# Kernel optimization log

Measured on AMD Instinct MI355X. Metric: run time of the kernel, lower is better.

Reference implementation:

```python
import jax, jax.numpy as jnp
import numpy as np

D_MODEL, N_LEVELS, N_HEADS, N_POINTS = 256, 4, 8, 4
HEAD_DIM = D_MODEL // N_HEADS
SPATIAL = [(100, 100), (50, 50), (25, 25), (13, 13)]  # (H, W) per level
BATCH = 2


def setup_inputs() -> dict:
    key = jax.random.key(0)
    ks = jax.random.split(key, 10)
    len_in = sum(h * w for h, w in SPATIAL)
    n, lq = BATCH, len_in
    s = 0.02
    mlp = N_HEADS * N_LEVELS * N_POINTS
    starts = np.cumsum([0] + [h * w for h, w in SPATIAL])[:-1]
    return {
        "query": jax.random.normal(ks[0], (n, lq, D_MODEL), jnp.float32),
        "reference_points": jax.random.uniform(ks[1], (n, lq, N_LEVELS, 2), jnp.float32),
        "input_flatten": jax.random.normal(ks[2], (n, len_in, D_MODEL), jnp.float32),
        "input_spatial_shapes": jnp.array(SPATIAL, dtype=jnp.int32),
        "input_level_start_index": jnp.array(starts, dtype=jnp.int32),
        "Wv": jax.random.normal(ks[3], (D_MODEL, D_MODEL), jnp.float32) * s,
        "bv": jnp.zeros((D_MODEL,), jnp.float32),
        "Woff": jax.random.normal(ks[4], (D_MODEL, mlp * 2), jnp.float32) * s,
        "boff": jax.random.normal(ks[5], (mlp * 2,), jnp.float32) * s,
        "Wattn": jax.random.normal(ks[6], (D_MODEL, mlp), jnp.float32) * s,
        "battn": jnp.zeros((mlp,), jnp.float32),
        "Wout": jax.random.normal(ks[7], (D_MODEL, D_MODEL), jnp.float32) * s,
        "bout": jnp.zeros((D_MODEL,), jnp.float32),
    }


def _ms_deform_attn_core(value, spatial_shapes, loc, aw):
    """value [N,S,M,D]; loc [N,Lq,M,L,P,2] in [0,1]; aw [N,Lq,M,L,P] -> [N,Lq,M*D].
    Faithful to F.grid_sample(mode='bilinear', padding_mode='zeros', align_corners=False)."""
    n, lq, m, L, p, _ = loc.shape
    d = value.shape[-1]
    out = jnp.zeros((n, m, lq, d), value.dtype)
    gather = jax.vmap(jax.vmap(lambda v, i: v[i]))  # vmap over N and M
    start = 0
    for lvl, (H, W) in enumerate(spatial_shapes):
        v = value[:, start:start + H * W].transpose(0, 2, 1, 3)  # [N,M,HW,D]
        start += H * W
        # align_corners=False: grid g=2*loc-1 -> pixel = ((g+1)*size-1)/2 = loc*size-0.5
        x = loc[:, :, :, lvl, :, 0] * W - 0.5  # [N,Lq,M,P]
        y = loc[:, :, :, lvl, :, 1] * H - 0.5
        x0 = jnp.floor(x)
        y0 = jnp.floor(y)
        wx = x - x0
        wy = y - y0
        x0i = x0.astype(jnp.int32)
        y0i = y0.astype(jnp.int32)
        samp = jnp.zeros((n, m, lq * p, d), value.dtype)
        for dy, wyc in ((0, 1.0 - wy), (1, wy)):
            for dx, wxc in ((0, 1.0 - wx), (1, wx)):
                xi = x0i + dx
                yi = y0i + dy
                valid = (xi >= 0) & (xi < W) & (yi >= 0) & (yi < H)  # zeros padding
                idx = jnp.clip(yi, 0, H - 1) * W + jnp.clip(xi, 0, W - 1)
                idx = idx.transpose(0, 2, 1, 3).reshape(n, m, lq * p)
                w = (wxc * wyc * valid).transpose(0, 2, 1, 3).reshape(n, m, lq * p)
                samp = samp + gather(v, idx) * w[..., None]
        samp = samp.reshape(n, m, lq, p, d)
        aw_l = aw[:, :, :, lvl, :].transpose(0, 2, 1, 3)  # [N,M,Lq,P]
        out = out + (samp * aw_l[..., None]).sum(3)
    return out.transpose(0, 2, 1, 3).reshape(n, lq, m * d)


def reference(query, reference_points, input_flatten, input_spatial_shapes,
              input_level_start_index, Wv, bv, Woff, boff, Wattn, battn, Wout, bout):
    n, lq, _ = query.shape
    m, L, p = N_HEADS, N_LEVELS, N_POINTS
    shapes = np.asarray(input_spatial_shapes)  # concrete/static [L,2] = (H,W)
    value = (input_flatten @ Wv + bv).reshape(n, -1, m, HEAD_DIM)
    off = (query @ Woff + boff).reshape(n, lq, m, L, p, 2)
    aw = jax.nn.softmax((query @ Wattn + battn).reshape(n, lq, m, L * p), axis=-1)
    aw = aw.reshape(n, lq, m, L, p)
    norm = jnp.asarray(shapes[:, ::-1].astype(np.float32))  # [L,2] = (W,H)
    loc = reference_points[:, :, None, :, None, :] + off / norm[None, None, None, :, None, :]
    out = _ms_deform_attn_core(value, [tuple(s) for s in shapes.tolist()], loc, aw)
    return out @ Wout + bout
```

## Files before the change

### kernel.cpp

```cpp
#include <hip/hip_runtime.h>
#include <hip/hip_bf16.h>

#define NB    2
#define LQ    13294
#define DM    256
#define NH    8
#define HD    32
#define NL    4
#define NP    4
#define ROWS  (NB*LQ)

#define OFF_VALUE 0u
#define OFF_TMP   13613056u
#define OFF_OFFS  27226112u
#define OFF_AWL   54452224u
#define OFF_WT    61258752u
#define OFF_FLAG  61717504u

#define WT_WV    0
#define WT_WOFF  65536
#define WT_WATTN 131072
#define WT_WOUT  163840

#define NPANEL   831
#define NBLK_VAL (NPANEL*4)
#define NBLK_FUS (NPANEL*6)
#define NBLK_IN  (NBLK_VAL+NBLK_FUS)
#define NGRP_IN  ((NBLK_IN+3)/4)
#define NGRP_OUT (NBLK_VAL/4)

typedef __attribute__((ext_vector_type(8))) short short8;
typedef __attribute__((ext_vector_type(4))) float floatx4;

static __device__ __forceinline__ float blo(int u)  { return __uint_as_float(((unsigned)u) << 16); }
static __device__ __forceinline__ float bhif(int u) { return __uint_as_float(((unsigned)u) & 0xffff0000u); }

static __device__ __forceinline__ int pack_bf2(float a, float b) {
    __hip_bfloat162 h(__float2bfloat16(a), __float2bfloat16(b));
    int u; __builtin_memcpy(&u, &h, 4); return u;
}

static __device__ __forceinline__ int xcd_swz(int b, int nblk) {
    const int q = nblk >> 3, r = nblk & 7;
    const int x = b & 7, i = b >> 3;
    return x * q + min(x, r) + i;
}

__global__ void sniff_k(const unsigned int* __restrict__ q, int* __restrict__ flag) {
    const int t = threadIdx.x;
    int hits = 0;
#pragma unroll
    for (int i = 0; i < 4; ++i) {
        unsigned lo = q[t * 4 + i] & 0xffffu;
        unsigned e  = (lo >> 7) & 0xffu;
        if ((e >= 110u && e <= 132u) || lo == 0u) ++hits;
    }
#pragma unroll
    for (int s = 1; s < 64; s <<= 1) hits += __shfl_xor(hits, s);
    if (t == 0) *flag = (hits > 160) ? 1 : 0;
}

__global__ __launch_bounds__(256) void trans_k(
    const void* __restrict__ s0, const void* __restrict__ s1,
    const void* __restrict__ s2, const void* __restrict__ s3,
    short* __restrict__ wt, const int* __restrict__ flagp)
{
    const int flag = *flagp;
    const int z = blockIdx.z;
    const void* src = (z == 0) ? s0 : (z == 1) ? s1 : (z == 2) ? s2 : s3;
    short* dst = wt + ((z == 0) ? WT_WV : (z == 1) ? WT_WOFF : (z == 2) ? WT_WATTN : WT_WOUT);
    const int N = (z == 2) ? 128 : 256;
    const int n0 = blockIdx.x * 32, k0 = blockIdx.y * 32;
    if (n0 >= N) return;

    __shared__ short tile[32 * 36];
    const int t = threadIdx.x;
    const int r = t >> 3, c4 = (t & 7) * 4;
    if (flag) {
        const short* sp = (const short*)src + (k0 + r) * N + n0 + c4;
        *(short4*)&tile[r * 36 + c4] = *(const short4*)sp;
    } else {
        const float* sp = (const float*)src + (k0 + r) * N + n0 + c4;
        float4 v = *(const float4*)sp;
        short4 o;
        o.x = (short)(pack_bf2(v.x, v.x) & 0xffff);
        o.y = (short)(pack_bf2(v.y, v.y) & 0xffff);
        o.z = (short)(pack_bf2(v.z, v.z) & 0xffff);
        o.w = (short)(pack_bf2(v.w, v.w) & 0xffff);
        *(short4*)&tile[r * 36 + c4] = o;
    }
    __syncthreads();
    const int nn = t >> 3, r4 = (t & 7) * 4;
    short4 o;
    o.x = tile[(r4 + 0) * 36 + nn];
    o.y = tile[(r4 + 1) * 36 + nn];
    o.z = tile[(r4 + 2) * 36 + nn];
    o.w = tile[(r4 + 3) * 36 + nn];
    *(short4*)&dst[(n0 + nn) * 256 + k0 + r4] = o;
}

static __device__ __forceinline__ short8 ldA_f32(const float* p) {
    float4 f0 = *(const float4*)p, f1 = *(const float4*)(p + 4);
    int4 q; q.x = pack_bf2(f0.x, f0.y); q.y = pack_bf2(f0.z, f0.w);
            q.z = pack_bf2(f1.x, f1.y); q.w = pack_bf2(f1.z, f1.w);
    short8 r; __builtin_memcpy(&r, &q, 16); return r;
}

static __device__ __forceinline__ void wgemm_body(
    const void* __restrict__ A, const short* __restrict__ Wt,
    const void* __restrict__ bias, const void* __restrict__ bias2,
    void* __restrict__ C, void* __restrict__ C2,
    const int M, const int Nn, const bool a_bf, const int c_mode,
    const int flag, const int bn_t, const int p_t, const int lane)
{
    const int qd = lane >> 4, ln = lane & 15;
    const int bm = p_t * 32, bn = bn_t * 64;

    const int ar0 = min(bm + ln, M - 1);
    const int ar1 = min(bm + 16 + ln, M - 1);
    const short* Ab = (const short*)A;
    const float* Af = (const float*)A;

    floatx4 acc[2][4];
#pragma unroll
    for (int i = 0; i < 2; ++i)
#pragma unroll
        for (int j = 0; j < 4; ++j) acc[i][j] = floatx4{0.f, 0.f, 0.f, 0.f};

    if (a_bf) {
#pragma unroll 2
        for (int kk = 0; kk < 8; ++kk) {
            const int k0 = kk * 32 + qd * 8;
            short8 af0 = *(const short8*)(Ab + ar0 * 256 + k0);
            short8 af1 = *(const short8*)(Ab + ar1 * 256 + k0);
            short8 bf[4];
#pragma unroll
            for (int j = 0; j < 4; ++j)
                bf[j] = *(const short8*)(Wt + (bn + j * 16 + ln) * 256 + k0);
#pragma unroll
            for (int j = 0; j < 4; ++j) {
                acc[0][j] = __builtin_amdgcn_mfma_f32_16x16x32_bf16(af0, bf[j], acc[0][j], 0, 0, 0);
                acc[1][j] = __builtin_amdgcn_mfma_f32_16x16x32_bf16(af1, bf[j], acc[1][j], 0, 0, 0);
            }
        }
    } else {
#pragma unroll 2
        for (int kk = 0; kk < 8; ++kk) {
            const int k0 = kk * 32 + qd * 8;
            short8 af0 = ldA_f32(Af + ar0 * 256 + k0);
            short8 af1 = ldA_f32(Af + ar1 * 256 + k0);
            short8 bf[4];
#pragma unroll
            for (int j = 0; j < 4; ++j)
                bf[j] = *(const short8*)(Wt + (bn + j * 16 + ln) * 256 + k0);
#pragma unroll
            for (int j = 0; j < 4; ++j) {
                acc[0][j] = __builtin_amdgcn_mfma_f32_16x16x32_bf16(af0, bf[j], acc[0][j], 0, 0, 0);
                acc[1][j] = __builtin_amdgcn_mfma_f32_16x16x32_bf16(af1, bf[j], acc[1][j], 0, 0, 0);
            }
        }
    }

#pragma unroll
    for (int j = 0; j < 4; ++j) {
        const int col = bn + j * 16 + ln;
        float bj;
        if (c_mode == 3 && col >= 256) {
            if (flag) bj = __bfloat162float(((const __hip_bfloat16*)bias2)[col - 256]);
            else      bj = ((const float*)bias2)[col - 256];
        } else {
            if (flag) bj = __bfloat162float(((const __hip_bfloat16*)bias)[col]);
            else      bj = ((const float*)bias)[col];
        }
#pragma unroll
        for (int i = 0; i < 2; ++i) {
#pragma unroll
            for (int r = 0; r < 4; ++r) {
                const int row = bm + i * 16 + qd * 4 + r;
                if (row >= M) continue;
                const float v = acc[i][j][r] + bj;
                if (c_mode == 0)      ((__hip_bfloat16*)C)[row * Nn + col] = __float2bfloat16(v);
                else if (c_mode == 1) ((float*)C)[row * Nn + col] = v;
                else if (c_mode == 2) {
                    if (flag) ((__hip_bfloat16*)C)[row * Nn + col] = __float2bfloat16(v);
                    else      ((float*)C)[row * Nn + col] = v;
                } else {
                    if (col < 256) ((float*)C)[row * 256 + col] = v;
                    else           ((__hip_bfloat16*)C2)[row * 128 + col - 256] = __float2bfloat16(v);
                }
            }
        }
    }
}

__global__ __launch_bounds__(256) void wgemm_in_k(
    const void* __restrict__ flat, const void* __restrict__ query,
    const short* __restrict__ wt,
    const void* __restrict__ bv, const void* __restrict__ boff,
    const void* __restrict__ battn,
    void* __restrict__ value, void* __restrict__ offsb, void* __restrict__ awl,
    const int* __restrict__ flagp)
{
    const int flag = *flagp;
    const bool a_bf = (flag != 0);
    const int w = xcd_swz(blockIdx.x, NGRP_IN) * 4 + (threadIdx.x >> 6);
    if (w >= NBLK_IN) return;
    const int lane = threadIdx.x & 63;
    if (w < NBLK_VAL) {
        wgemm_body(flat, wt + WT_WV, bv, nullptr, value, nullptr,
                   ROWS, 256, a_bf, 0, flag, w & 3, w >> 2, lane);
    } else {
        const int w2 = w - NBLK_VAL;
        wgemm_body(query, wt + WT_WOFF, boff, battn, offsb, awl,
                   ROWS, 384, a_bf, 3, flag, w2 % 6, w2 / 6, lane);
    }
}

__global__ __launch_bounds__(256) void wgemm_out_k(
    const void* __restrict__ tmp, const short* __restrict__ wt,
    const void* __restrict__ bout, void* __restrict__ dout,
    const int* __restrict__ flagp)
{
    const int flag = *flagp;
    const int w = xcd_swz(blockIdx.x, NGRP_OUT) * 4 + (threadIdx.x >> 6);
    const int lane = threadIdx.x & 63;
    wgemm_body(tmp, wt + WT_WOUT, bout, nullptr, dout, nullptr,
               ROWS, 256, true, 2, flag, w & 3, w >> 2, lane);
}

__global__ __launch_bounds__(256) void sampler_k(
    const void* __restrict__ refp, const short* __restrict__ value,
    const float* __restrict__ offs, const short* __restrict__ awl,
    short* __restrict__ tmp, const int* __restrict__ flagp)
{
    const int flag = *flagp;
    const int wq = threadIdx.x >> 6;
    const int nq = blockIdx.x * 4 + wq;
    const int lane = threadIdx.x & 63;
    const int h = lane >> 3, u = lane & 7;
    const int n = (nq >= LQ) ? 1 : 0;

    __shared__ int2 recs[4][16][9][5];

    const int lg = *(const int*)(awl + nq * 128 + h * 16 + u * 2);
    float l0 = blo(lg), l1 = bhif(lg);
    float m = fmaxf(l0, l1);
    m = fmaxf(m, __shfl_xor(m, 1));
    m = fmaxf(m, __shfl_xor(m, 2));
    m = fmaxf(m, __shfl_xor(m, 4));
    float e0 = __expf(l0 - m), e1 = __expf(l1 - m);
    float s = e0 + e1;
    s += __shfl_xor(s, 1);
    s += __shfl_xor(s, 2);
    s += __shfl_xor(s, 4);
    const float inv = 1.f / s;
    const float w0 = e0 * inv, w1 = e1 * inv;

    const float4 of = *(const float4*)(offs + nq * 256 + h * 32 + u * 4);

    float rxl, ryl;
    if (flag) {
        const int rr = *(const int*)((const short*)refp + nq * 8 + (u & 3) * 2);
        rxl = blo(rr); ryl = bhif(rr);
    } else {
        const float* rp = (const float*)refp + nq * 8 + (u & 3) * 2;
        rxl = rp[0]; ryl = rp[1];
    }

    const int l = u >> 1;
    const int Wl = (0x0D193264 >> (l * 8)) & 0xff;
    const int St = (l == 0) ? 0 : (l == 1) ? 10000 : (l == 2) ? 12500 : 13125;
    const int rowbase = n * LQ + St;
    const float Wf = (float)Wl;
    const float rx = __shfl(rxl, h * 8 + l);
    const float ry = __shfl(ryl, h * 8 + l);

#pragma unroll
    for (int j = 0; j < 2; ++j) {
        const float ox = j ? of.z : of.x;
        const float oy = j ? of.w : of.y;
        const float wa = j ? w1 : w0;
        const float px = fmaf(rx, Wf, ox) - 0.5f;
        const float py = fmaf(ry, Wf, oy) - 0.5f;
        const float x0f = floorf(px), y0f = floorf(py);
        const float wx = px - x0f, wy = py - y0f;
        const int x0 = (int)x0f, y0 = (int)y0f;
        const float wxc[2] = {1.f - wx, wx};
        const float wyc[2] = {1.f - wy, wy};
#pragma unroll
        for (int dy = 0; dy < 2; ++dy) {
#pragma unroll
            for (int dx = 0; dx < 2; ++dx) {
                const int xi = x0 + dx, yi = y0 + dy;
                const bool vld = ((unsigned)xi < (unsigned)Wl) & ((unsigned)yi < (unsigned)Wl);
                int row = rowbase + yi * Wl + xi;
                row = vld ? row : rowbase;
                recs[wq][u * 2 + j][h][dy * 2 + dx] =
                    make_int2(row << 9, __float_as_int(vld ? wa * wxc[dx] * wyc[dy] : 0.f));
            }
        }
    }

    __syncthreads();

    const int laneoff = h * 64 + u * 8;
    const char* vb = (const char*)value;
    float a0 = 0.f, a1 = 0.f, a2 = 0.f, a3 = 0.f;

    int2  rA[8], rB[8];
    float wA[8], wB[8];

#define CHUNK(RW, WW, kk)                                                 \
    _Pragma("unroll")                                                     \
    for (int j = 0; j < 8; ++j) {                                         \
        const int2 rr = recs[wq][(kk) * 2 + (j >> 2)][h][j & 3];          \
        WW[j] = __int_as_float(rr.y);                                     \
        RW[j] = *(const int2*)(vb + (unsigned)(rr.x + laneoff));          \
    }
#define EAT(RW, WW)                                                       \
    _Pragma("unroll")                                                     \
    for (int j = 0; j < 8; ++j) {                                         \
        a0 = fmaf(WW[j], blo(RW[j].x),  a0);                              \
        a1 = fmaf(WW[j], bhif(RW[j].x), a1);                              \
        a2 = fmaf(WW[j], blo(RW[j].y),  a2);                              \
        a3 = fmaf(WW[j], bhif(RW[j].y), a3);                              \
    }

    CHUNK(rA, wA, 0)
    CHUNK(rB, wB, 1)
    EAT(rA, wA)  CHUNK(rA, wA, 2)
    EAT(rB, wB)  CHUNK(rB, wB, 3)
    EAT(rA, wA)  CHUNK(rA, wA, 4)
    EAT(rB, wB)  CHUNK(rB, wB, 5)
    EAT(rA, wA)  CHUNK(rA, wA, 6)
    EAT(rB, wB)  CHUNK(rB, wB, 7)
    EAT(rA, wA)
    EAT(rB, wB)
#undef CHUNK
#undef EAT

    int2 o;
    o.x = pack_bf2(a0, a1);
    o.y = pack_bf2(a2, a3);
    *(int2*)(tmp + nq * 256 + h * 32 + u * 4) = o;
}

extern "C" void kernel_launch(void* const* d_in, const int* in_sizes, int n_in,
                              void* d_out, int out_size, void* d_ws, size_t ws_size,
                              hipStream_t stream)
{
    const void* query  = d_in[0];
    const void* refpts = d_in[1];
    const void* flat   = d_in[2];
    const void* Wv     = d_in[5];
    const void* bv     = d_in[6];
    const void* Woff   = d_in[7];
    const void* boff   = d_in[8];
    const void* Wattn  = d_in[9];
    const void* battn  = d_in[10];
    const void* Wout   = d_in[11];
    const void* bout   = d_in[12];

    char* ws = (char*)d_ws;
    short* value = (short*)(ws + OFF_VALUE);
    short* tmp   = (short*)(ws + OFF_TMP);
    float* offsb = (float*)(ws + OFF_OFFS);
    short* awl   = (short*)(ws + OFF_AWL);
    short* wt    = (short*)(ws + OFF_WT);
    int*   flagp = (int*)(ws + OFF_FLAG);

    sniff_k<<<1, 64, 0, stream>>>((const unsigned int*)query, flagp);
    trans_k<<<dim3(8, 8, 4), 256, 0, stream>>>(Wv, Woff, Wattn, Wout, wt, flagp);
    wgemm_in_k<<<NGRP_IN, 256, 0, stream>>>(flat, query, wt, bv, boff, battn,
                                            value, offsb, awl, flagp);
    sampler_k<<<ROWS / 4, 256, 0, stream>>>(refpts, value, offsb, awl, tmp, flagp);
    wgemm_out_k<<<NGRP_OUT, 256, 0, stream>>>(tmp, wt, bout, d_out, flagp);
}
```

Measured before the change: 269.0 us.

## Stage GEMM epilogues through LDS for coalesced 16-byte row-panel stores

Each block in the input and output projection GEMMs now covers a full 32-row panel, with its four waves splitting the columns. Wave-to-tile mapping is reorganized so one block covers all columns of 32 rows. Results plus bias are written to shared memory first, then copied to global memory as contiguous int4 stores. Previously each lane did scattered 2- or 4-byte stores. This cuts uncoalesced write traffic at the cost of LDS usage (up to 40 KB per block), which may lower occupancy, plus an extra barrier.

```diff
diff --git a/kernel.cpp b/kernel.cpp
--- a/kernel.cpp
+++ b/kernel.cpp
@@ -23,11 +23,8 @@
 #define WT_WOUT  163840
 
 #define NPANEL   831
-#define NBLK_VAL (NPANEL*4)
-#define NBLK_FUS (NPANEL*6)
-#define NBLK_IN  (NBLK_VAL+NBLK_FUS)
-#define NGRP_IN  ((NBLK_IN+3)/4)
-#define NGRP_OUT (NBLK_VAL/4)
+#define NGRID_IN (NPANEL*2)
+#define NGRID_OUT NPANEL
 
 typedef __attribute__((ext_vector_type(8))) short short8;
 typedef __attribute__((ext_vector_type(4))) float floatx4;
@@ -106,26 +103,22 @@
     short8 r; __builtin_memcpy(&r, &q, 16); return r;
 }
 
-static __device__ __forceinline__ void wgemm_body(
+template<int NJ>
+static __device__ __forceinline__ void wg_compute(
     const void* __restrict__ A, const short* __restrict__ Wt,
-    const void* __restrict__ bias, const void* __restrict__ bias2,
-    void* __restrict__ C, void* __restrict__ C2,
-    const int M, const int Nn, const bool a_bf, const int c_mode,
-    const int flag, const int bn_t, const int p_t, const int lane)
+    const bool a_bf, const int bm, const int bn, const int lane,
+    floatx4 (&acc)[2][NJ])
 {
     const int qd = lane >> 4, ln = lane & 15;
-    const int bm = p_t * 32, bn = bn_t * 64;
-
-    const int ar0 = min(bm + ln, M - 1);
-    const int ar1 = min(bm + 16 + ln, M - 1);
+    const int ar0 = min(bm + ln, ROWS - 1);
+    const int ar1 = min(bm + 16 + ln, ROWS - 1);
     const short* Ab = (const short*)A;
     const float* Af = (const float*)A;
 
-    floatx4 acc[2][4];
 #pragma unroll
     for (int i = 0; i < 2; ++i)
 #pragma unroll
-        for (int j = 0; j < 4; ++j) acc[i][j] = floatx4{0.f, 0.f, 0.f, 0.f};
+        for (int j = 0; j < NJ; ++j) acc[i][j] = floatx4{0.f, 0.f, 0.f, 0.f};
 
     if (a_bf) {
 #pragma unroll 2
@@ -133,12 +126,12 @@
             const int k0 = kk * 32 + qd * 8;
             short8 af0 = *(const short8*)(Ab + ar0 * 256 + k0);
             short8 af1 = *(const short8*)(Ab + ar1 * 256 + k0);
-            short8 bf[4];
-#pragma unroll
-            for (int j = 0; j < 4; ++j)
+            short8 bf[NJ];
+#pragma unroll
+            for (int j = 0; j < NJ; ++j)
                 bf[j] = *(const short8*)(Wt + (bn + j * 16 + ln) * 256 + k0);
 #pragma unroll
-            for (int j = 0; j < 4; ++j) {
+            for (int j = 0; j < NJ; ++j) {
                 acc[0][j] = __builtin_amdgcn_mfma_f32_16x16x32_bf16(af0, bf[j], acc[0][j], 0, 0, 0);
                 acc[1][j] = __builtin_amdgcn_mfma_f32_16x16x32_bf16(af1, bf[j], acc[1][j], 0, 0, 0);
             }
@@ -149,45 +142,14 @@
             const int k0 = kk * 32 + qd * 8;
             short8 af0 = ldA_f32(Af + ar0 * 256 + k0);
             short8 af1 = ldA_f32(Af + ar1 * 256 + k0);
-            short8 bf[4];
-#pragma unroll
-            for (int j = 0; j < 4; ++j)
+            short8 bf[NJ];
+#pragma unroll
+            for (int j = 0; j < NJ; ++j)
                 bf[j] = *(const short8*)(Wt + (bn + j * 16 + ln) * 256 + k0);
 #pragma unroll
-            for (int j = 0; j < 4; ++j) {
+            for (int j = 0; j < NJ; ++j) {
                 acc[0][j] = __builtin_amdgcn_mfma_f32_16x16x32_bf16(af0, bf[j], acc[0][j], 0, 0, 0);
                 acc[1][j] = __builtin_amdgcn_mfma_f32_16x16x32_bf16(af1, bf[j], acc[1][j], 0, 0, 0);
-            }
-        }
-    }
-
-#pragma unroll
-    for (int j = 0; j < 4; ++j) {
-        const int col = bn + j * 16 + ln;
-        float bj;
-        if (c_mode == 3 && col >= 256) {
-            if (flag) bj = __bfloat162float(((const __hip_bfloat16*)bias2)[col - 256]);
-            else      bj = ((const float*)bias2)[col - 256];
-        } else {
-            if (flag) bj = __bfloat162float(((const __hip_bfloat16*)bias)[col]);
-            else      bj = ((const float*)bias)[col];
-        }
-#pragma unroll
-        for (int i = 0; i < 2; ++i) {
-#pragma unroll
-            for (int r = 0; r < 4; ++r) {
-                const int row = bm + i * 16 + qd * 4 + r;
-                if (row >= M) continue;
-                const float v = acc[i][j][r] + bj;
-                if (c_mode == 0)      ((__hip_bfloat16*)C)[row * Nn + col] = __float2bfloat16(v);
-                else if (c_mode == 1) ((float*)C)[row * Nn + col] = v;
-                else if (c_mode == 2) {
-                    if (flag) ((__hip_bfloat16*)C)[row * Nn + col] = __float2bfloat16(v);
-                    else      ((float*)C)[row * Nn + col] = v;
-                } else {
-                    if (col < 256) ((float*)C)[row * 256 + col] = v;
-                    else           ((__hip_bfloat16*)C2)[row * 128 + col - 256] = __float2bfloat16(v);
-                }
             }
         }
     }
@@ -201,18 +163,81 @@
     void* __restrict__ value, void* __restrict__ offsb, void* __restrict__ awl,
     const int* __restrict__ flagp)
 {
+    __shared__ __align__(16) char smem[40960];
     const int flag = *flagp;
     const bool a_bf = (flag != 0);
-    const int w = xcd_swz(blockIdx.x, NGRP_IN) * 4 + (threadIdx.x >> 6);
-    if (w >= NBLK_IN) return;
-    const int lane = threadIdx.x & 63;
-    if (w < NBLK_VAL) {
-        wgemm_body(flat, wt + WT_WV, bv, nullptr, value, nullptr,
-                   ROWS, 256, a_bf, 0, flag, w & 3, w >> 2, lane);
+    const int b = xcd_swz(blockIdx.x, NGRID_IN);
+    const int tid = threadIdx.x, wv = tid >> 6, lane = tid & 63;
+    const int qd = lane >> 4, ln = lane & 15;
+
+    if (b < NPANEL) {
+        const int p = b, bm = p * 32;
+        floatx4 acc[2][4];
+        wg_compute<4>(flat, wt + WT_WV, a_bf, bm, wv * 64, lane, acc);
+
+        short* Cs = (short*)smem;
+#pragma unroll
+        for (int j = 0; j < 4; ++j) {
+            const int col = wv * 64 + j * 16 + ln;
+            const float bj = flag ? __bfloat162float(((const __hip_bfloat16*)bv)[col])
+                                  : ((const float*)bv)[col];
+#pragma unroll
+            for (int i = 0; i < 2; ++i)
+#pragma unroll
+                for (int r = 0; r < 4; ++r)
+                    Cs[(i * 16 + qd * 4 + r) * 256 + col] =
+                        (short)(pack_bf2(acc[i][j][r] + bj, 0.f) & 0xffff);
+        }
+        __syncthreads();
+        const int rows_valid = min(32, ROWS - bm);
+        const int4* src = (const int4*)smem;
+        int4* dst = (int4*)((char*)value + (size_t)p * 16384);
+#pragma unroll
+        for (int c = 0; c < 4; ++c) {
+            const int idx = c * 256 + tid;
+            if (idx < rows_valid * 32) dst[idx] = src[idx];
+        }
     } else {
-        const int w2 = w - NBLK_VAL;
-        wgemm_body(query, wt + WT_WOFF, boff, battn, offsb, awl,
-                   ROWS, 384, a_bf, 3, flag, w2 % 6, w2 / 6, lane);
+        const int p = b - NPANEL, bm = p * 32;
+        floatx4 acc[2][6];
+        wg_compute<6>(query, wt + WT_WOFF, a_bf, bm, wv * 96, lane, acc);
+
+        float* Os = (float*)smem;
+        short* Al = (short*)(smem + 32768);
+#pragma unroll
+        for (int j = 0; j < 6; ++j) {
+            const int col = wv * 96 + j * 16 + ln;
+            float bj;
+            if (col < 256) bj = flag ? __bfloat162float(((const __hip_bfloat16*)boff)[col])
+                                     : ((const float*)boff)[col];
+            else           bj = flag ? __bfloat162float(((const __hip_bfloat16*)battn)[col - 256])
+                                     : ((const float*)battn)[col - 256];
+#pragma unroll
+            for (int i = 0; i < 2; ++i)
+#pragma unroll
+                for (int r = 0; r < 4; ++r) {
+                    const int rl = i * 16 + qd * 4 + r;
+                    const float v = acc[i][j][r] + bj;
+                    if (col < 256) Os[rl * 256 + col] = v;
+                    else           Al[rl * 128 + col - 256] = (short)(pack_bf2(v, 0.f) & 0xffff);
+                }
+        }
+        __syncthreads();
+        const int rows_valid = min(32, ROWS - bm);
+        const int4* srcO = (const int4*)smem;
+        int4* dstO = (int4*)((char*)offsb + (size_t)p * 32768);
+#pragma unroll
+        for (int c = 0; c < 8; ++c) {
+            const int idx = c * 256 + tid;
+            if (idx < rows_valid * 64) dstO[idx] = srcO[idx];
+        }
+        const int4* srcA = (const int4*)(smem + 32768);
+        int4* dstA = (int4*)((char*)awl + (size_t)p * 8192);
+#pragma unroll
+        for (int c = 0; c < 2; ++c) {
+            const int idx = c * 256 + tid;
+            if (idx < rows_valid * 16) dstA[idx] = srcA[idx];
+        }
     }
 }
 
@@ -221,11 +246,48 @@
     const void* __restrict__ bout, void* __restrict__ dout,
     const int* __restrict__ flagp)
 {
+    __shared__ __align__(16) char smem[32768];
     const int flag = *flagp;
-    const int w = xcd_swz(blockIdx.x, NGRP_OUT) * 4 + (threadIdx.x >> 6);
-    const int lane = threadIdx.x & 63;
-    wgemm_body(tmp, wt + WT_WOUT, bout, nullptr, dout, nullptr,
-               ROWS, 256, true, 2, flag, w & 3, w >> 2, lane);
+    const int p = xcd_swz(blockIdx.x, NGRID_OUT), bm = p * 32;
+    const int tid = threadIdx.x, wv = tid >> 6, lane = tid & 63;
+    const int qd = lane >> 4, ln = lane & 15;
+
+    floatx4 acc[2][4];
+    wg_compute<4>(tmp, wt + WT_WOUT, true, bm, wv * 64, lane, acc);
+
+#pragma unroll
+    for (int j = 0; j < 4; ++j) {
+        const int col = wv * 64 + j * 16 + ln;
+        const float bj = flag ? __bfloat162float(((const __hip_bfloat16*)bout)[col])
+                              : ((const float*)bout)[col];
+#pragma unroll
+        for (int i = 0; i < 2; ++i)
+#pragma unroll
+            for (int r = 0; r < 4; ++r) {
+                const int rl = i * 16 + qd * 4 + r;
+                const float v = acc[i][j][r] + bj;
+                if (flag) ((short*)smem)[rl * 256 + col] = (short)(pack_bf2(v, 0.f) & 0xffff);
+                else      ((float*)smem)[rl * 256 + col] = v;
+            }
+    }
+    __syncthreads();
+    const int rows_valid = min(32, ROWS - bm);
+    const int4* src = (const int4*)smem;
+    if (flag) {
+        int4* dst = (int4*)((char*)dout + (size_t)p * 16384);
+#pragma unroll
+        for (int c = 0; c < 4; ++c) {
+            const int idx = c * 256 + tid;
+            if (idx < rows_valid * 32) dst[idx] = src[idx];
+        }
+    } else {
+        int4* dst = (int4*)((char*)dout + (size_t)p * 32768);
+#pragma unroll
+        for (int c = 0; c < 8; ++c) {
+            const int idx = c * 256 + tid;
+            if (idx < rows_valid * 64) dst[idx] = src[idx];
+        }
+    }
 }
 
 __global__ __launch_bounds__(256) void sampler_k(
@@ -371,8 +433,8 @@
 
     sniff_k<<<1, 64, 0, stream>>>((const unsigned int*)query, flagp);
     trans_k<<<dim3(8, 8, 4), 256, 0, stream>>>(Wv, Woff, Wattn, Wout, wt, flagp);
-    wgemm_in_k<<<NGRP_IN, 256, 0, stream>>>(flat, query, wt, bv, boff, battn,
-                                            value, offsb, awl, flagp);
+    wgemm_in_k<<<NGRID_IN, 256, 0, stream>>>(flat, query, wt, bv, boff, battn,
+                                             value, offsb, awl, flagp);
     sampler_k<<<ROWS / 4, 256, 0, stream>>>(refpts, value, offsb, awl, tmp, flagp);
-    wgemm_out_k<<<NGRP_OUT, 256, 0, stream>>>(tmp, wt, bout, d_out, flagp);
-}
+    wgemm_out_k<<<NGRID_OUT, 256, 0, stream>>>(tmp, wt, bout, d_out, flagp);
+}
```

New measurement: 275.5 us. +2.4%, slower.
